# Kernel optimization log

Measured on AMD Instinct MI355X. Metric: run time of the kernel, lower is better.

Reference implementation:

```python
import jax, jax.numpy as jnp
import numpy as np
import math

B, S, E, H = 2, 1024, 2560, 32
D = E // H  # 80


def setup_inputs() -> dict:
    key = jax.random.key(0)
    ks = jax.random.split(key, 10)
    hidden_states = jax.random.normal(ks[0], (B, S, E), dtype=jnp.float32)
    Wqkv = jax.random.normal(ks[1], (E, 3 * E), dtype=jnp.float32) * 0.02
    bqkv = jnp.zeros((3 * E,), dtype=jnp.float32)
    Wproj = jax.random.normal(ks[2], (E, E), dtype=jnp.float32) * 0.02
    bproj = jnp.zeros((E,), dtype=jnp.float32)
    # gate matrices: hadamard, pauli_x, pauli_z (all real branches in torch code)
    hadamard = jnp.array([[1.0, 1.0], [1.0, -1.0]], dtype=jnp.float32) / math.sqrt(2.0)
    pauli_x = jnp.array([[0.0, 1.0], [1.0, 0.0]], dtype=jnp.float32)
    pauli_z = jnp.array([[1.0, 0.0], [0.0, -1.0]], dtype=jnp.float32)
    gate_mats = jnp.stack([hadamard, pauli_x, pauli_z])  # (3,2,2)
    # phase_rotation init is zeros in torch; randomize slightly for nontrivial numerics
    gate_phases = jax.random.normal(ks[3], (3, D), dtype=jnp.float32) * 0.1
    gate_amps = jnp.ones((3, D), dtype=jnp.float32)
    quantum_phase = jax.random.normal(ks[4], (H,), dtype=jnp.float32) * 0.1
    interference_strength = jnp.float32(0.8)
    return {
        'hidden_states': hidden_states, 'Wqkv': Wqkv, 'bqkv': bqkv,
        'Wproj': Wproj, 'bproj': bproj, 'gate_mats': gate_mats,
        'gate_phases': gate_phases, 'gate_amps': gate_amps,
        'quantum_phase': quantum_phase,
        'interference_strength': interference_strength,
    }


def _gate_coeffs(gate_mats, gate_phases, gate_amps):
    # QuantumGate fwd: stack([x*cos(p), x*sin(p)], -1) @ G, summed over last axis, * amp
    # => per-dim scalar coeff: (cos(p)*(g00+g01) + sin(p)*(g10+g11)) * amp
    row0 = gate_mats[:, 0, 0] + gate_mats[:, 0, 1]  # (3,)
    row1 = gate_mats[:, 1, 0] + gate_mats[:, 1, 1]  # (3,)
    return (jnp.cos(gate_phases) * row0[:, None] + jnp.sin(gate_phases) * row1[:, None]) * gate_amps  # (3, D)


def reference(hidden_states, Wqkv, bqkv, Wproj, bproj, gate_mats, gate_phases, gate_amps, quantum_phase, interference_strength):
    scale = D ** -0.5
    qkv = hidden_states @ Wqkv + bqkv  # (B,S,3E)
    q, k, v = jnp.split(qkv, 3, axis=-1)
    # (B,H,S,D)
    q = q.reshape(B, S, H, D).transpose(0, 2, 1, 3)
    k = k.reshape(B, S, H, D).transpose(0, 2, 1, 3)
    v = v.reshape(B, S, H, D).transpose(0, 2, 1, 3)

    attn_scores = jnp.einsum('bhqd,bhkd->bhqk', q, k) * scale

    coeffs = _gate_coeffs(gate_mats, gate_phases, gate_amps)  # (3,D)
    # quantum attention per gate: (q * coeff_i) @ k^T * scale
    qa = jnp.einsum('gd,bhqd,bhkd->gbhqk', coeffs, q, k) * scale  # (3,B,H,S,S)
    interference = (qa[0] * qa[1] + qa[0] * qa[2] + qa[1] * qa[2]) * interference_strength
    attn_scores = attn_scores + interference / 3.0

    attn_probs = jax.nn.softmax(attn_scores, axis=-1)
    attn_probs = attn_probs * jnp.cos(quantum_phase)[None, :, None, None]

    attn_output = jnp.einsum('bhqk,bhkd->bhqd', attn_probs, v)
    attn_output = attn_output.transpose(0, 2, 1, 3).reshape(B, S, E)
    return attn_output @ Wproj + bproj
```

## Files before the change

kernel.cpp:

```cpp
#include <hip/hip_runtime.h>
#include <hip/hip_bf16.h>
#include <math.h>

#define S_  1024
#define E_  2560
#define H_  32
#define D_  80
#define E3_ 7680
#define M_  2048
#define QK_ 5120

typedef short bf16x8 __attribute__((ext_vector_type(8)));
typedef float f32x4  __attribute__((ext_vector_type(4)));

static __device__ __forceinline__ float bf2f(unsigned short u) {
    unsigned int i = ((unsigned int)u) << 16;
    float f; __builtin_memcpy(&f, &i, 4); return f;
}
static __device__ __forceinline__ unsigned short f2bf(float f) {
    unsigned int i; __builtin_memcpy(&i, &f, 4);
    i += 0x7fffu + ((i >> 16) & 1u);
    return (unsigned short)(i >> 16);
}

static __device__ __forceinline__ void gload_lds16(
    const unsigned short* g, unsigned short* l)
{
    __builtin_amdgcn_global_load_lds(
        (const __attribute__((address_space(1))) void*)g,
        (__attribute__((address_space(3))) void*)l, 16, 0, 0);
}

__global__ __launch_bounds__(256) void cvt_bf16_kernel(
    const float* __restrict__ in, unsigned short* __restrict__ out, int n8)
{
    int i = (blockIdx.x * 256 + threadIdx.x);
    if (i >= n8) return;
    const float* p = in + (size_t)i * 8;
    float4 a = *(const float4*)p;
    float4 b = *(const float4*)(p + 4);
    union { uint4 v; unsigned short s[8]; } o;
    o.s[0]=f2bf(a.x); o.s[1]=f2bf(a.y); o.s[2]=f2bf(a.z); o.s[3]=f2bf(a.w);
    o.s[4]=f2bf(b.x); o.s[5]=f2bf(b.y); o.s[6]=f2bf(b.z); o.s[7]=f2bf(b.w);
    *(uint4*)(out + (size_t)i * 8) = o.v;
}

__global__ __launch_bounds__(256) void transpose_bf16_kernel(
    const float* __restrict__ in, unsigned short* __restrict__ out, int R, int C)
{
    const int t = threadIdx.x;
    const int r0 = blockIdx.y * 64, c0 = blockIdx.x * 64;
    const int r4 = (t >> 4) * 4;
    const int c4 = (t & 15) * 4;
    float4 rows[4];
#pragma unroll
    for (int i = 0; i < 4; ++i)
        rows[i] = *(const float4*)&in[(size_t)(r0 + r4 + i) * C + c0 + c4];
    const float rv[4][4] = {
        {rows[0].x, rows[0].y, rows[0].z, rows[0].w},
        {rows[1].x, rows[1].y, rows[1].z, rows[1].w},
        {rows[2].x, rows[2].y, rows[2].z, rows[2].w},
        {rows[3].x, rows[3].y, rows[3].z, rows[3].w}};
#pragma unroll
    for (int j = 0; j < 4; ++j) {
        ushort4 o;
        o.x = f2bf(rv[0][j]); o.y = f2bf(rv[1][j]);
        o.z = f2bf(rv[2][j]); o.w = f2bf(rv[3][j]);
        *(ushort4*)&out[(size_t)(c0 + c4 + j) * R + r0 + r4] = o;
    }
}

template <bool OUT_F32>
__global__ __launch_bounds__(256) void mfma_gemm_kernel(
    const unsigned short* __restrict__ A, int lda,
    const unsigned short* __restrict__ Wt,
    const float* __restrict__ bias,
    void* __restrict__ dst0, int sd0,
    void* __restrict__ dst1, int sd1, int ncut,
    int K)
{
    __shared__ unsigned short As[2][128 * 32];
    __shared__ unsigned short Bs[2][128 * 32];
    const int BUFSZ = 128 * 32;

    const int t    = threadIdx.x;
    const int m0   = blockIdx.y * 128;
    const int n0   = blockIdx.x * 128;
    const int lane = t & 63, wave = t >> 6;
    const int quad = lane >> 4, l15 = lane & 15;
    const int mw   = (wave >> 1) * 64;
    const int nw   = (wave & 1) * 64;

    f32x4 acc[4][4];
#pragma unroll
    for (int i = 0; i < 4; ++i)
#pragma unroll
        for (int j = 0; j < 4; ++j) acc[i][j] = (f32x4){0.f, 0.f, 0.f, 0.f};

    const int srow  = lane >> 2;
    const int sslot = (lane & 3) * 8;

    const unsigned short* gA0 = A  + (size_t)(m0 + wave * 32 + srow) * lda + sslot;
    const unsigned short* gA1 = gA0 + (size_t)16 * lda;
    const unsigned short* gB0 = Wt + (size_t)(n0 + wave * 32 + srow) * K + sslot;
    const unsigned short* gB1 = gB0 + (size_t)16 * K;
    unsigned short* lA0 = &As[0][(wave * 32) * 32];
    unsigned short* lA1 = lA0 + 16 * 32;
    unsigned short* lB0 = &Bs[0][(wave * 32) * 32];
    unsigned short* lB1 = lB0 + 16 * 32;

    gload_lds16(gA0, lA0);
    gload_lds16(gA1, lA1);
    gload_lds16(gB0, lB0);
    gload_lds16(gB1, lB1);
    __syncthreads();

    int cur = 0;
    for (int k0 = 0; k0 < K; k0 += 32) {
        const int nxt = cur ^ 1;
        if (k0 + 32 < K) {
            gload_lds16(gA0 + k0 + 32, lA0 + nxt * BUFSZ);
            gload_lds16(gA1 + k0 + 32, lA1 + nxt * BUFSZ);
            gload_lds16(gB0 + k0 + 32, lB0 + nxt * BUFSZ);
            gload_lds16(gB1 + k0 + 32, lB1 + nxt * BUFSZ);
        }

        const unsigned short* rA = &As[cur][0];
        const unsigned short* rB = &Bs[cur][0];
        bf16x8 af[4], bfr[4];
#pragma unroll
        for (int i = 0; i < 4; ++i)
            af[i] = *(const bf16x8*)&rA[(mw + i * 16 + l15) * 32 + quad * 8];
#pragma unroll
        for (int j = 0; j < 4; ++j)
            bfr[j] = *(const bf16x8*)&rB[(nw + j * 16 + l15) * 32 + quad * 8];
#pragma unroll
        for (int i = 0; i < 4; ++i)
#pragma unroll
            for (int j = 0; j < 4; ++j)
                acc[i][j] = __builtin_amdgcn_mfma_f32_16x16x32_bf16(af[i], bfr[j], acc[i][j], 0, 0, 0);

        __syncthreads();
        cur = nxt;
    }

#pragma unroll
    for (int j = 0; j < 4; ++j) {
        const int col = n0 + nw + j * 16 + l15;
        const float bv = bias[col];
        if (OUT_F32) {
            float* dst = (float*)dst0;
#pragma unroll
            for (int i = 0; i < 4; ++i) {
                const int rowb = m0 + mw + i * 16 + quad * 4;
#pragma unroll
                for (int g = 0; g < 4; ++g)
                    dst[(size_t)(rowb + g) * sd0 + col] = acc[i][j][g] + bv;
            }
        } else {
            unsigned short* dst; int sd, cc;
            if (col < ncut) { dst = (unsigned short*)dst0; sd = sd0; cc = col; }
            else            { dst = (unsigned short*)dst1; sd = sd1; cc = col - ncut; }
#pragma unroll
            for (int i = 0; i < 4; ++i) {
                const int rowb = m0 + mw + i * 16 + quad * 4;
#pragma unroll
                for (int g = 0; g < 4; ++g)
                    dst[(size_t)(rowb + g) * sd + cc] = f2bf(acc[i][j][g] + bv);
            }
        }
    }
}

__global__ __launch_bounds__(256, 2) void attn_mfma_kernel(
    unsigned short* __restrict__ qk,
    const unsigned short* __restrict__ vsrc,
    const float* __restrict__ gmats,
    const float* __restrict__ gphases,
    const float* __restrict__ gamps,
    const float* __restrict__ qphase,
    const float* __restrict__ is_ptr)
{
    __shared__ unsigned short Ks[64 * 104];
    __shared__ unsigned short Vt[80 * 72];
    __shared__ unsigned short Ps[64 * 72];
    __shared__ float cs[240];

    const int t    = threadIdx.x;
    const int wave = t >> 6, lane = t & 63;
    const int quad = lane >> 4, l15 = lane & 15;
    const int lin0 = blockIdx.x;
    const int lin  = ((lin0 & 7) << 7) | (lin0 >> 3);
    const int qt = lin & 15;
    const int bh = lin >> 4;
    const int h  = bh & 31;
    const int b  = bh >> 5;

    const float scale = 0.111803398874989485f;
    const float c2    = scale * scale * is_ptr[0] * (1.0f / 3.0f);
    const float cosph = cosf(qphase[h]);

    if (t < 240) {
        int g = t / 80;
        float r0 = gmats[g*4+0] + gmats[g*4+1];
        float r1 = gmats[g*4+2] + gmats[g*4+3];
        cs[t] = (cosf(gphases[t]) * r0 + sinf(gphases[t]) * r1) * gamps[t];
    }

    const int srow = t >> 2;
    const int scg  = (t & 3) * 20;

    {
        const unsigned short* qp = qk + (size_t)(b * S_ + qt * 64 + srow) * QK_ + h * D_ + scg;
#pragma unroll
        for (int u = 0; u < 5; ++u)
            *(ushort4*)&Ks[srow * 104 + scg + 4 * u] = *(const ushort4*)(qp + 4 * u);
        *(ushort4*)&Ks[srow * 104 + 80 + (t & 3) * 4] = (ushort4){0, 0, 0, 0};
    }
    __syncthreads();

    bf16x8 afq[3], afg[3][3];
#pragma unroll
    for (int kc = 0; kc < 3; ++kc)
        afq[kc] = *(const bf16x8*)&Ks[(wave * 16 + l15) * 104 + quad * 8 + kc * 32];
#pragma unroll
    for (int g = 0; g < 3; ++g)
#pragma unroll
        for (int kc = 0; kc < 3; ++kc)
#pragma unroll
            for (int j = 0; j < 8; ++j) {
                int d = kc * 32 + quad * 8 + j;
                float c = (d < 80) ? cs[g * 80 + d] : 0.f;
                afg[g][kc][j] = (short)f2bf(bf2f((unsigned short)afq[kc][j]) * c);
            }

    f32x4 Ov[5];
#pragma unroll
    for (int nf = 0; nf < 5; ++nf) Ov[nf] = (f32x4){0.f, 0.f, 0.f, 0.f};
    float m_r[4] = {-INFINITY, -INFINITY, -INFINITY, -INFINITY};
    float l_r[4] = {0.f, 0.f, 0.f, 0.f};

    for (int kt = 0; kt < 16; ++kt) {
        __syncthreads();

        const unsigned short* kp = qk + (size_t)(b * S_ + kt * 64 + srow) * QK_ + E_ + h * D_ + scg;
#pragma unroll
        for (int u = 0; u < 5; ++u)
            *(ushort4*)&Ks[srow * 104 + scg + 4 * u] = *(const ushort4*)(kp + 4 * u);

        for (int s = t; s < 320; s += 256) {
            const int vkg = s & 15, vdg = s >> 4;
            ushort4 rv[4];
#pragma unroll
            for (int i = 0; i < 4; ++i)
                rv[i] = *(const ushort4*)&vsrc[(size_t)(b * S_ + kt * 64 + vkg * 4 + i) * E_ + h * D_ + vdg * 4];
            const unsigned short rm[4][4] = {
                {rv[0].x, rv[0].y, rv[0].z, rv[0].w},
                {rv[1].x, rv[1].y, rv[1].z, rv[1].w},
                {rv[2].x, rv[2].y, rv[2].z, rv[2].w},
                {rv[3].x, rv[3].y, rv[3].z, rv[3].w}};
#pragma unroll
            for (int j = 0; j < 4; ++j) {
                ushort4 w = {rm[0][j], rm[1][j], rm[2][j], rm[3][j]};
                *(ushort4*)&Vt[(vdg * 4 + j) * 72 + vkg * 4] = w;
            }
        }
        __syncthreads();

        float p[4][4];
        float mx[4] = {-INFINITY, -INFINITY, -INFINITY, -INFINITY};
#pragma unroll
        for (int hf = 0; hf < 2; ++hf) {
            f32x4 sacc[4][2];
#pragma unroll
            for (int v = 0; v < 4; ++v)
#pragma unroll
                for (int n = 0; n < 2; ++n) sacc[v][n] = (f32x4){0.f, 0.f, 0.f, 0.f};
#pragma unroll
            for (int kc = 0; kc < 3; ++kc) {
                bf16x8 bk[2];
#pragma unroll
                for (int n = 0; n < 2; ++n)
                    bk[n] = *(const bf16x8*)&Ks[((hf * 2 + n) * 16 + l15) * 104 + quad * 8 + kc * 32];
#pragma unroll
                for (int n = 0; n < 2; ++n)
                    sacc[0][n] = __builtin_amdgcn_mfma_f32_16x16x32_bf16(afq[kc], bk[n], sacc[0][n], 0, 0, 0);
#pragma unroll
                for (int g = 0; g < 3; ++g)
#pragma unroll
                    for (int n = 0; n < 2; ++n)
                        sacc[1+g][n] = __builtin_amdgcn_mfma_f32_16x16x32_bf16(afg[g][kc], bk[n], sacc[1+g][n], 0, 0, 0);
            }
#pragma unroll
            for (int n = 0; n < 2; ++n)
#pragma unroll
                for (int r = 0; r < 4; ++r) {
                    float s0 = sacc[1][n][r], s1 = sacc[2][n][r], s2 = sacc[3][n][r];
                    float s = fmaf(fmaf(s0, s1, (s0 + s1) * s2), c2, sacc[0][n][r] * scale);
                    p[hf * 2 + n][r] = s;
                    mx[r] = fmaxf(mx[r], s);
                }
        }

#pragma unroll
        for (int r = 0; r < 4; ++r) {
            mx[r] = fmaxf(mx[r], __shfl_xor(mx[r], 1));
            mx[r] = fmaxf(mx[r], __shfl_xor(mx[r], 2));
            mx[r] = fmaxf(mx[r], __shfl_xor(mx[r], 4));
            mx[r] = fmaxf(mx[r], __shfl_xor(mx[r], 8));
        }
        float alpha[4];
#pragma unroll
        for (int r = 0; r < 4; ++r) {
            float m_new = fmaxf(m_r[r], mx[r]);
            alpha[r] = __expf(m_r[r] - m_new);
            m_r[r] = m_new;
        }
#pragma unroll
        for (int nf = 0; nf < 4; ++nf)
#pragma unroll
            for (int r = 0; r < 4; ++r)
                p[nf][r] = __expf(p[nf][r] - m_r[r]);
#pragma unroll
        for (int r = 0; r < 4; ++r) {
            float s = p[0][r] + p[1][r] + p[2][r] + p[3][r];
            s += __shfl_xor(s, 1);
            s += __shfl_xor(s, 2);
            s += __shfl_xor(s, 4);
            s += __shfl_xor(s, 8);
            l_r[r] = l_r[r] * alpha[r] + s;
        }

#pragma unroll
        for (int nf = 0; nf < 4; ++nf)
#pragma unroll
            for (int r = 0; r < 4; ++r)
                Ps[(wave * 16 + quad * 4 + r) * 72 + l15 + 16 * nf] = f2bf(p[nf][r]);
        __asm__ volatile("s_waitcnt lgkmcnt(0)" ::: "memory");

#pragma unroll
        for (int nf = 0; nf < 5; ++nf)
#pragma unroll
            for (int r = 0; r < 4; ++r) Ov[nf][r] *= alpha[r];

        bf16x8 ap[2];
#pragma unroll
        for (int kc = 0; kc < 2; ++kc)
            ap[kc] = *(const bf16x8*)&Ps[(wave * 16 + l15) * 72 + quad * 8 + kc * 32];
#pragma unroll
        for (int nf = 0; nf < 5; ++nf)
#pragma unroll
            for (int kc = 0; kc < 2; ++kc) {
                bf16x8 bv = *(const bf16x8*)&Vt[(nf * 16 + l15) * 72 + quad * 8 + kc * 32];
                Ov[nf] = __builtin_amdgcn_mfma_f32_16x16x32_bf16(ap[kc], bv, Ov[nf], 0, 0, 0);
            }
    }

    float inv[4];
#pragma unroll
    for (int r = 0; r < 4; ++r) inv[r] = cosph / l_r[r];
#pragma unroll
    for (int nf = 0; nf < 5; ++nf)
#pragma unroll
        for (int r = 0; r < 4; ++r)
            qk[(size_t)(b * S_ + qt * 64 + wave * 16 + quad * 4 + r) * QK_ + h * D_ + nf * 16 + l15]
                = f2bf(Ov[nf][r] * inv[r]);
}

extern "C" void kernel_launch(void* const* d_in, const int* in_sizes, int n_in,
                              void* d_out, int out_size, void* d_ws, size_t ws_size,
                              hipStream_t stream) {
    (void)in_sizes; (void)n_in; (void)out_size; (void)ws_size;
    const float* hidden  = (const float*)d_in[0];
    const float* Wqkv    = (const float*)d_in[1];
    const float* bqkv    = (const float*)d_in[2];
    const float* Wproj   = (const float*)d_in[3];
    const float* bproj   = (const float*)d_in[4];
    const float* gmats   = (const float*)d_in[5];
    const float* gphases = (const float*)d_in[6];
    const float* gamps   = (const float*)d_in[7];
    const float* qphase  = (const float*)d_in[8];
    const float* is_ptr  = (const float*)d_in[9];

    unsigned short* qk_ws  = (unsigned short*)d_ws;
    unsigned short* h_bf16 = (unsigned short*)((char*)d_ws + (size_t)M_ * QK_ * 2);
    unsigned short* Wt     = (unsigned short*)((char*)d_ws + (size_t)M_ * QK_ * 2 + (size_t)M_ * E_ * 2);
    unsigned short* v_buf  = (unsigned short*)d_out;

    dim3 blk(256);
    cvt_bf16_kernel<<<dim3((M_ * E_ / 8 + 255) / 256), blk, 0, stream>>>(hidden, h_bf16, M_ * E_ / 8);
    transpose_bf16_kernel<<<dim3(E3_/64, E_/64), blk, 0, stream>>>(Wqkv, Wt, E_, E3_);
    mfma_gemm_kernel<false><<<dim3(E3_/128, M_/128), blk, 0, stream>>>(
        h_bf16, E_, Wt, bqkv, qk_ws, QK_, v_buf, E_, QK_, E_);
    attn_mfma_kernel<<<dim3(2 * H_ * (S_/64)), blk, 0, stream>>>(
        qk_ws, v_buf, gmats, gphases, gamps, qphase, is_ptr);
    transpose_bf16_kernel<<<dim3(E_/64, E_/64), blk, 0, stream>>>(Wproj, Wt, E_, E_);
    mfma_gemm_kernel<true><<<dim3(E_/128, M_/128), blk, 0, stream>>>(
        qk_ws, QK_, Wt, bproj, d_out, E_, d_out, E_, E_, E_);
}
```

Measured before the change: 470.1 us.

## Prefetch next K/V tile into registers during attention compute

The attention loop now loads the next K tile and V tile from global memory into registers (kpre/vpre) right after the LDS barrier, so these loads overlap the current tile's score, softmax and PV work. At the start of each iteration the registers are written to LDS, with V transposed as before, instead of loading and storing in one step. The V loop over 320 slots is unrolled into one fixed slot per thread plus an extra slot for threads below 64. This adds about 26 VGPRs of prefetch state, which may lower occupancy.

Result: faster. 455.6 us (-3.1%).

```diff
diff --git a/kernel.cpp b/kernel.cpp
--- a/kernel.cpp
+++ b/kernel.cpp
@@ -210,6 +210,9 @@
     const int srow = t >> 2;
     const int scg  = (t & 3) * 20;
 
+    const int vkg  = t & 15;
+    const int vdg0 = t >> 4;
+
     {
         const unsigned short* qp = qk + (size_t)(b * S_ + qt * 64 + srow) * QK_ + h * D_ + scg;
 #pragma unroll
@@ -218,6 +221,23 @@
         *(ushort4*)&Ks[srow * 104 + 80 + (t & 3) * 4] = (ushort4){0, 0, 0, 0};
     }
     __syncthreads();
+
+    ushort4 kpre[5];
+    ushort4 vpre[8];
+    {
+        const unsigned short* kp = qk + (size_t)(b * S_ + srow) * QK_ + E_ + h * D_ + scg;
+#pragma unroll
+        for (int u = 0; u < 5; ++u) kpre[u] = *(const ushort4*)(kp + 4 * u);
+        const unsigned short* vb = vsrc + (size_t)(b * S_) * E_ + h * D_;
+#pragma unroll
+        for (int i = 0; i < 4; ++i)
+            vpre[i] = *(const ushort4*)(vb + (size_t)(vkg * 4 + i) * E_ + vdg0 * 4);
+        if (t < 64) {
+#pragma unroll
+            for (int i = 0; i < 4; ++i)
+                vpre[4 + i] = *(const ushort4*)(vb + (size_t)(vkg * 4 + i) * E_ + 64 + vdg0 * 4);
+        }
+    }
 
     bf16x8 afq[3], afg[3][3];
 #pragma unroll
@@ -243,29 +263,50 @@
     for (int kt = 0; kt < 16; ++kt) {
         __syncthreads();
 
-        const unsigned short* kp = qk + (size_t)(b * S_ + kt * 64 + srow) * QK_ + E_ + h * D_ + scg;
 #pragma unroll
         for (int u = 0; u < 5; ++u)
-            *(ushort4*)&Ks[srow * 104 + scg + 4 * u] = *(const ushort4*)(kp + 4 * u);
-
-        for (int s = t; s < 320; s += 256) {
-            const int vkg = s & 15, vdg = s >> 4;
-            ushort4 rv[4];
-#pragma unroll
-            for (int i = 0; i < 4; ++i)
-                rv[i] = *(const ushort4*)&vsrc[(size_t)(b * S_ + kt * 64 + vkg * 4 + i) * E_ + h * D_ + vdg * 4];
+            *(ushort4*)&Ks[srow * 104 + scg + 4 * u] = kpre[u];
+
+        {
             const unsigned short rm[4][4] = {
-                {rv[0].x, rv[0].y, rv[0].z, rv[0].w},
-                {rv[1].x, rv[1].y, rv[1].z, rv[1].w},
-                {rv[2].x, rv[2].y, rv[2].z, rv[2].w},
-                {rv[3].x, rv[3].y, rv[3].z, rv[3].w}};
+                {vpre[0].x, vpre[0].y, vpre[0].z, vpre[0].w},
+                {vpre[1].x, vpre[1].y, vpre[1].z, vpre[1].w},
+                {vpre[2].x, vpre[2].y, vpre[2].z, vpre[2].w},
+                {vpre[3].x, vpre[3].y, vpre[3].z, vpre[3].w}};
 #pragma unroll
             for (int j = 0; j < 4; ++j) {
                 ushort4 w = {rm[0][j], rm[1][j], rm[2][j], rm[3][j]};
-                *(ushort4*)&Vt[(vdg * 4 + j) * 72 + vkg * 4] = w;
+                *(ushort4*)&Vt[(vdg0 * 4 + j) * 72 + vkg * 4] = w;
+            }
+        }
+        if (t < 64) {
+            const unsigned short rm[4][4] = {
+                {vpre[4].x, vpre[4].y, vpre[4].z, vpre[4].w},
+                {vpre[5].x, vpre[5].y, vpre[5].z, vpre[5].w},
+                {vpre[6].x, vpre[6].y, vpre[6].z, vpre[6].w},
+                {vpre[7].x, vpre[7].y, vpre[7].z, vpre[7].w}};
+#pragma unroll
+            for (int j = 0; j < 4; ++j) {
+                ushort4 w = {rm[0][j], rm[1][j], rm[2][j], rm[3][j]};
+                *(ushort4*)&Vt[(64 + vdg0 * 4 + j) * 72 + vkg * 4] = w;
             }
         }
         __syncthreads();
+
+        if (kt < 15) {
+            const unsigned short* kp = qk + (size_t)(b * S_ + (kt + 1) * 64 + srow) * QK_ + E_ + h * D_ + scg;
+#pragma unroll
+            for (int u = 0; u < 5; ++u) kpre[u] = *(const ushort4*)(kp + 4 * u);
+            const unsigned short* vb = vsrc + (size_t)(b * S_ + (kt + 1) * 64) * E_ + h * D_;
+#pragma unroll
+            for (int i = 0; i < 4; ++i)
+                vpre[i] = *(const ushort4*)(vb + (size_t)(vkg * 4 + i) * E_ + vdg0 * 4);
+            if (t < 64) {
+#pragma unroll
+                for (int i = 0; i < 4; ++i)
+                    vpre[4 + i] = *(const ushort4*)(vb + (size_t)(vkg * 4 + i) * E_ + 64 + vdg0 * 4);
+            }
+        }
 
         float p[4][4];
         float mx[4] = {-INFINITY, -INFINITY, -INFINITY, -INFINITY};
```
